# Performance work log

Hardware: AMD Instinct MI355X
Metric: run time of the kernel (lower is better)

The kernel has to match this reference:

```python
import jax, jax.numpy as jnp
import numpy as np

B, PS, D, HEADS, HD, PROP = 16, 32, 768, 8, 24, 4
N = PS * PS          # 1024 tokens
M = PROP * PROP      # 16 proposal centers
INNER = HEADS * HD   # 192
HID = 4 * D          # 3072
EPS = 1e-12


def setup_inputs() -> dict:
    key = jax.random.key(0)
    ks = jax.random.split(key, 8)
    s = 0.02
    f32 = jnp.float32
    return {
        "x": jax.random.normal(ks[0], (B, N, D), f32),
        "ln1_w": jnp.ones((D,), f32), "ln1_b": jnp.zeros((D,), f32),
        "f_w": jax.random.normal(ks[1], (INNER, D), f32) * s, "f_b": jnp.zeros((INNER,), f32),
        "v_w": jax.random.normal(ks[2], (INNER, D), f32) * s, "v_b": jnp.zeros((INNER,), f32),
        "proj_w": jax.random.normal(ks[3], (D, INNER), f32) * s, "proj_b": jnp.zeros((D,), f32),
        "sim_alpha": jnp.ones((1,), f32), "sim_beta": jnp.zeros((1,), f32),
        "ln2_w": jnp.ones((D,), f32), "ln2_b": jnp.zeros((D,), f32),
        "fc1_w": jax.random.normal(ks[4], (HID, D), f32) * s, "fc1_b": jnp.zeros((HID,), f32),
        "fc2_w": jax.random.normal(ks[5], (D, HID), f32) * s, "fc2_b": jnp.zeros((D,), f32),
    }


def _ln(x, w, b):
    mu = x.mean(-1, keepdims=True)
    var = ((x - mu) ** 2).mean(-1, keepdims=True)
    return (x - mu) / jnp.sqrt(var + 1e-5) * w + b


def _cluster2d(x, f_w, f_b, v_w, v_b, proj_w, proj_b, alpha, beta):
    b = x.shape[0]
    xi = x.reshape(b, PS, PS, D).transpose(0, 3, 1, 2)  # b c w h
    # 1x1 convs f and v
    f = jnp.einsum('oc,bcwh->bowh', f_w, xi) + f_b[None, :, None, None]
    v = jnp.einsum('oc,bcwh->bowh', v_w, xi) + v_b[None, :, None, None]
    # split heads: (b e) c w h
    f = f.reshape(b * HEADS, HD, PS, PS)
    v = v.reshape(b * HEADS, HD, PS, PS)
    # adaptive avg pool to (PROP, PROP) -- exact kernel/stride pooling since PS % PROP == 0
    s = PS // PROP
    cen = f.reshape(-1, HD, PROP, s, PROP, s).mean((3, 5))  # be c 4 4
    vcen = v.reshape(-1, HD, PROP, s, PROP, s).mean((3, 5)).reshape(-1, HD, M).transpose(0, 2, 1)  # be M c
    cf = cen.reshape(-1, HD, M).transpose(0, 2, 1)  # be M c
    xf = f.reshape(-1, HD, N).transpose(0, 2, 1)    # be N c
    # pairwise euclidean similarity on L2-normalized vectors: ||a-b|| = sqrt(2 - 2 a.b)
    cn = cf / jnp.maximum(jnp.linalg.norm(cf, axis=-1, keepdims=True), EPS)
    xn = xf / jnp.maximum(jnp.linalg.norm(xf, axis=-1, keepdims=True), EPS)
    dist = jnp.sqrt(jnp.clip(2.0 - 2.0 * jnp.einsum('bmc,bnc->bmn', cn, xn), EPS, None))
    sim = jax.nn.leaky_relu(beta + alpha * jnp.exp(-dist), 0.2)  # be M N (dropout eval = identity)
    # top-1 hard assignment (torch scatter of argmax -> one-hot mask, no grad through mask)
    mask = jax.nn.one_hot(jnp.argmax(sim, axis=1), M, dtype=sim.dtype).transpose(0, 2, 1)  # be M N
    sim = sim * mask
    v2 = v.reshape(-1, HD, N).transpose(0, 2, 1)  # be N c
    # weighted reduce to centers, then broadcast back to tokens
    outc = (jnp.einsum('bmn,bnc->bmc', sim, v2) + vcen) / (mask.sum(-1, keepdims=True) + 1.0)  # be M c
    out = jnp.einsum('bmn,bmc->bnc', sim, outc)  # be N c
    out = out.reshape(-1, PS, PS, HD).transpose(0, 3, 1, 2).reshape(b, INNER, PS, PS)
    out = jnp.einsum('oc,bcwh->bowh', proj_w, out) + proj_b[None, :, None, None]
    return out.transpose(0, 2, 3, 1).reshape(b, N, D)


def reference(x, ln1_w, ln1_b, f_w, f_b, v_w, v_b, proj_w, proj_b, sim_alpha, sim_beta,
              ln2_w, ln2_b, fc1_w, fc1_b, fc2_w, fc2_b):
    h = x + _cluster2d(_ln(x, ln1_w, ln1_b), f_w, f_b, v_w, v_b, proj_w, proj_b, sim_alpha, sim_beta)
    y = _ln(h, ln2_w, ln2_b)
    y = jax.nn.gelu(jnp.einsum('bnd,hd->bnh', y, fc1_w) + fc1_b, approximate=False)
    y = jnp.einsum('bnh,dh->bnd', y, fc2_w) + fc2_b
    return h + y
```

## Files before the change

### kernel.cpp

```cpp
#include <hip/hip_runtime.h>
#include <hip/hip_bf16.h>
#include <cmath>

typedef unsigned short u16;
typedef short short8 __attribute__((ext_vector_type(8)));
typedef float f32x4 __attribute__((ext_vector_type(4)));

#define D_ 768
#define NTOK 16384
#define INNER_ 192
#define HID_ 3072

__device__ __forceinline__ float u2f(u16 u) { return __uint_as_float((unsigned)u << 16); }
__device__ __forceinline__ u16 f2u(float f) {
  __hip_bfloat16 h = __float2bfloat16(f);
  u16 u; __builtin_memcpy(&u, &h, 2); return u;
}
__device__ __forceinline__ float ld1(const void* p, size_t i, int f32) {
  return f32 ? ((const float*)p)[i] : u2f(((const u16*)p)[i]);
}
__device__ __forceinline__ void st1(void* p, size_t i, float v, int f32) {
  if (f32) ((float*)p)[i] = v; else ((u16*)p)[i] = f2u(v);
}
__device__ __forceinline__ float gelu_exact(float v) {
  return 0.5f * v * (1.f + erff(v * 0.7071067811865476f));
}
__device__ __forceinline__ void unpack8(const uint4 v, float* o) {
  o[0] = u2f((u16)(v.x & 0xffffu)); o[1] = u2f((u16)(v.x >> 16));
  o[2] = u2f((u16)(v.y & 0xffffu)); o[3] = u2f((u16)(v.y >> 16));
  o[4] = u2f((u16)(v.z & 0xffffu)); o[5] = u2f((u16)(v.z >> 16));
  o[6] = u2f((u16)(v.w & 0xffffu)); o[7] = u2f((u16)(v.w >> 16));
}

__global__ __launch_bounds__(64) void detect_kernel(const unsigned* __restrict__ x,
                                                    int* __restrict__ flag) {
  int cnt = 0;
  for (int i = threadIdx.x; i < 512; i += 64) {
    const unsigned e0 = (x[i] >> 7) & 0xFFu;
    if (e0 >= 96u && e0 <= 144u) cnt++;
  }
#pragma unroll
  for (int o = 32; o > 0; o >>= 1) cnt += __shfl_down(cnt, o);
  if (threadIdx.x == 0) flag[0] = (cnt < 256) ? 1 : 0;
}

struct CvtJob { const void* src; u16* dst; int n4; };
struct CvtArgs { CvtJob j[10]; };

__global__ __launch_bounds__(256) void cvt_kernel(CvtArgs a, const int* __restrict__ flagp) {
  const int f32 = flagp[0];
  const CvtJob jb = a.j[blockIdx.y];
  const int i = blockIdx.x * 256 + threadIdx.x;
  if (i >= jb.n4) return;
  if (f32) {
    const float4 v = ((const float4*)jb.src)[i];
    const unsigned lo = (unsigned)f2u(v.x) | ((unsigned)f2u(v.y) << 16);
    const unsigned hi = (unsigned)f2u(v.z) | ((unsigned)f2u(v.w) << 16);
    ((uint2*)jb.dst)[i] = make_uint2(lo, hi);
  } else {
    ((uint2*)jb.dst)[i] = ((const uint2*)jb.src)[i];
  }
}

__global__ __launch_bounds__(256) void ln_kernel(const void* __restrict__ x,
                                                 const void* __restrict__ w,
                                                 const void* __restrict__ b,
                                                 u16* __restrict__ y,
                                                 const int* __restrict__ flagp) {
  const int fl = flagp[0];
  const size_t t = blockIdx.x;
  float v[3];
  float s = 0.f, s2 = 0.f;
#pragma unroll
  for (int i = 0; i < 3; i++) {
    v[i] = ld1(x, t * D_ + threadIdx.x + 256 * i, fl);
    s += v[i];
    s2 += v[i] * v[i];
  }
#pragma unroll
  for (int o = 32; o > 0; o >>= 1) {
    s += __shfl_down(s, o);
    s2 += __shfl_down(s2, o);
  }
  __shared__ float ps[4], ps2[4];
  __shared__ float smu, srstd;
  const int wid = threadIdx.x >> 6, lane = threadIdx.x & 63;
  if (lane == 0) { ps[wid] = s; ps2[wid] = s2; }
  __syncthreads();
  if (threadIdx.x == 0) {
    const float a = ps[0] + ps[1] + ps[2] + ps[3];
    const float a2 = ps2[0] + ps2[1] + ps2[2] + ps2[3];
    const float mu = a * (1.f / D_);
    smu = mu;
    srstd = rsqrtf(a2 * (1.f / D_) - mu * mu + 1e-5f);
  }
  __syncthreads();
  const float mu = smu, rstd = srstd;
#pragma unroll
  for (int i = 0; i < 3; i++) {
    const int c = threadIdx.x + 256 * i;
    y[t * D_ + c] = f2u((v[i] - mu) * rstd * ld1(w, c, fl) + ld1(b, c, fl));
  }
}

template <int EPI>
__global__ __launch_bounds__(256) void mfma_gemm(const u16* __restrict__ A, int lda,
                                                 const u16* __restrict__ B, int ldb,
                                                 const u16* __restrict__ bias,
                                                 const void* __restrict__ res,
                                                 void* __restrict__ C, int ldc,
                                                 int K, int row0,
                                                 const int* __restrict__ flagp) {
  const int fl = flagp[0];
  __shared__ __align__(16) u16 Asb[128 * 32];
  __shared__ __align__(16) u16 Bsb[128 * 32];
  const int tid = threadIdx.x;
  const int lane = tid & 63;
  const int wv = tid >> 6;
  const int bm = blockIdx.x * 128;
  const int bn = blockIdx.y * 128;
  const int wm = (wv & 1) * 64;
  const int wn = (wv >> 1) * 64;
  const int c0 = tid, c1 = tid + 256;
  const u16* Ag0 = A + (size_t)(bm + (c0 >> 2)) * lda + (c0 & 3) * 8;
  const u16* Ag1 = A + (size_t)(bm + (c1 >> 2)) * lda + (c1 & 3) * 8;
  const u16* Bg0 = B + (size_t)(bn + (c0 >> 2)) * ldb + (c0 & 3) * 8;
  const u16* Bg1 = B + (size_t)(bn + (c1 >> 2)) * ldb + (c1 & 3) * 8;
  u16* la0 = &Asb[c0 * 8];
  u16* la1 = &Asb[c1 * 8];
  u16* lb0 = &Bsb[c0 * 8];
  u16* lb1 = &Bsb[c1 * 8];

  f32x4 acc[4][4];
#pragma unroll
  for (int i = 0; i < 4; i++)
#pragma unroll
    for (int j = 0; j < 4; j++) acc[i][j] = (f32x4){0.f, 0.f, 0.f, 0.f};

  const int ml = lane & 15;
  const int kq = (lane >> 4) * 8;

  for (int k0 = 0; k0 < K; k0 += 32) {
    __syncthreads();
    __builtin_amdgcn_global_load_lds(
        (const __attribute__((address_space(1))) void*)(Ag0 + k0),
        (__attribute__((address_space(3))) void*)la0, 16, 0, 0);
    __builtin_amdgcn_global_load_lds(
        (const __attribute__((address_space(1))) void*)(Ag1 + k0),
        (__attribute__((address_space(3))) void*)la1, 16, 0, 0);
    __builtin_amdgcn_global_load_lds(
        (const __attribute__((address_space(1))) void*)(Bg0 + k0),
        (__attribute__((address_space(3))) void*)lb0, 16, 0, 0);
    __builtin_amdgcn_global_load_lds(
        (const __attribute__((address_space(1))) void*)(Bg1 + k0),
        (__attribute__((address_space(3))) void*)lb1, 16, 0, 0);
    __syncthreads();
    short8 af[4], bf[4];
#pragma unroll
    for (int i = 0; i < 4; i++) {
      af[i] = *(const short8*)&Asb[(wm + i * 16 + ml) * 32 + kq];
      bf[i] = *(const short8*)&Bsb[(wn + i * 16 + ml) * 32 + kq];
    }
#pragma unroll
    for (int i = 0; i < 4; i++)
#pragma unroll
      for (int j = 0; j < 4; j++)
        acc[i][j] = __builtin_amdgcn_mfma_f32_16x16x32_bf16(af[i], bf[j], acc[i][j], 0, 0, 0);
  }

  const int qr = (lane >> 4) * 4;
#pragma unroll
  for (int i = 0; i < 4; i++) {
#pragma unroll
    for (int j = 0; j < 4; j++) {
      const int colg = bn + wn + j * 16 + ml;
      const float bb = u2f(bias[colg]);
#pragma unroll
      for (int r = 0; r < 4; r++) {
        const size_t row = (size_t)row0 + bm + wm + i * 16 + qr + r;
        float v = acc[i][j][r] + bb;
        if (EPI == 1) v = gelu_exact(v);
        if (EPI == 2) {
          v += ld1(res, row * ldc + colg, fl);
          st1(C, row * ldc + colg, v, fl);
        } else {
          ((u16*)C)[row * ldc + colg] = f2u(v);
        }
      }
    }
  }
}

__global__ __launch_bounds__(512) void cluster_kernel(u16* __restrict__ FV,
                                                      const void* __restrict__ alpha_p,
                                                      const void* __restrict__ beta_p,
                                                      const int* __restrict__ flagp) {
  const int fl = flagp[0];
  const int be = blockIdx.x;
  const int b = be >> 3, e = be & 7;
  const int tid = threadIdx.x;
  const float alpha = ld1(alpha_p, 0, fl), beta = ld1(beta_p, 0, fl);

  __shared__ __align__(16) u16 S[1024 * 24];
  __shared__ float cn[16][24];
  __shared__ float vcen[16][24];
  __shared__ float outc[16][24];
  __shared__ float rcn[16];
  __shared__ int cnt[16];

  u16* Fg = FV + ((size_t)b * 1024) * 384 + e * 24;
  const u16* Vg = Fg + 192;

  for (int c = tid; c < 3072; c += 512) {
    const int n = c / 3, q = c - n * 3;
    *(uint4*)&S[n * 24 + q * 8] = *(const uint4*)(Fg + (size_t)n * 384 + q * 8);
  }
  if (tid < 16) cnt[tid] = 0;
  __syncthreads();

  for (int t = tid; t < 384; t += 512) {
    const int m = t / 24, ch = t - m * 24;
    const int pw = m >> 2, ph = m & 3;
    float sum = 0.f;
    for (int dw = 0; dw < 8; dw++) {
      const int base = (pw * 8 + dw) * 32 + ph * 8;
      for (int dh = 0; dh < 8; dh++) sum += u2f(S[(base + dh) * 24 + ch]);
    }
    cn[m][ch] = sum * (1.f / 64.f);
  }
  __syncthreads();
  if (tid < 16) {
    float s = 0.f;
    for (int ch = 0; ch < 24; ch++) { const float v = cn[tid][ch]; s += v * v; }
    rcn[tid] = 1.f / fmaxf(sqrtf(s), 1e-12f);
  }
  __syncthreads();

  const int na = tid, nb = tid + 512;
  float besta = -3.4e38f, bestb = -3.4e38f;
  int bma = 0, bmb = 0;
  {
    float xa[24], xb[24];
    const uint4* ra = (const uint4*)&S[na * 24];
    const uint4* rb = (const uint4*)&S[nb * 24];
#pragma unroll
    for (int q = 0; q < 3; q++) {
      unpack8(ra[q], &xa[q * 8]);
      unpack8(rb[q], &xb[q * 8]);
    }
    float ssa = 0.f, ssb = 0.f;
#pragma unroll
    for (int ch = 0; ch < 24; ch++) {
      ssa = fmaf(xa[ch], xa[ch], ssa);
      ssb = fmaf(xb[ch], xb[ch], ssb);
    }
    const float rna = 1.f / fmaxf(sqrtf(ssa), 1e-12f);
    const float rnb = 1.f / fmaxf(sqrtf(ssb), 1e-12f);
    for (int m = 0; m < 16; m++) {
      float da = 0.f, db = 0.f;
#pragma unroll
      for (int k = 0; k < 12; k++) {
        const float2 c = *(const float2*)&cn[m][2 * k];
        da = fmaf(c.x, xa[2 * k], da); da = fmaf(c.y, xa[2 * k + 1], da);
        db = fmaf(c.x, xb[2 * k], db); db = fmaf(c.y, xb[2 * k + 1], db);
      }
      const float rc = rcn[m];
      da *= rna * rc;
      db *= rnb * rc;
      const float dda = sqrtf(fmaxf(2.f - 2.f * da, 1e-12f));
      const float ddb = sqrtf(fmaxf(2.f - 2.f * db, 1e-12f));
      const float za = beta + alpha * expf(-dda);
      const float zb = beta + alpha * expf(-ddb);
      const float sa = (za >= 0.f) ? za : 0.2f * za;
      const float sb = (zb >= 0.f) ? zb : 0.2f * zb;
      if (sa > besta) { besta = sa; bma = m; }
      if (sb > bestb) { bestb = sb; bmb = m; }
    }
    atomicAdd(&cnt[bma], 1);
    atomicAdd(&cnt[bmb], 1);
  }
  __syncthreads();

  for (int c = tid; c < 3072; c += 512) {
    const int n = c / 3, q = c - n * 3;
    *(uint4*)&S[n * 24 + q * 8] = *(const uint4*)(Vg + (size_t)n * 384 + q * 8);
  }
  if (tid < 384) outc[tid / 24][tid - (tid / 24) * 24] = 0.f;
  __syncthreads();

  for (int t = tid; t < 384; t += 512) {
    const int m = t / 24, ch = t - m * 24;
    const int pw = m >> 2, ph = m & 3;
    float sum = 0.f;
    for (int dw = 0; dw < 8; dw++) {
      const int base = (pw * 8 + dw) * 32 + ph * 8;
      for (int dh = 0; dh < 8; dh++) sum += u2f(S[(base + dh) * 24 + ch]);
    }
    vcen[m][ch] = sum * (1.f / 64.f);
  }

  {
    float va[24], vb[24];
    const uint4* ra = (const uint4*)&S[na * 24];
    const uint4* rb = (const uint4*)&S[nb * 24];
#pragma unroll
    for (int q = 0; q < 3; q++) {
      unpack8(ra[q], &va[q * 8]);
      unpack8(rb[q], &vb[q * 8]);
    }
#pragma unroll
    for (int ch = 0; ch < 24; ch++) {
      atomicAdd(&outc[bma][ch], besta * va[ch]);
      atomicAdd(&outc[bmb][ch], bestb * vb[ch]);
    }
  }
  __syncthreads();

  for (int t = tid; t < 384; t += 512) {
    const int m = t / 24, ch = t - m * 24;
    outc[m][ch] = (outc[m][ch] + vcen[m][ch]) / ((float)cnt[m] + 1.f);
  }
  __syncthreads();

#pragma unroll
  for (int pass = 0; pass < 2; pass++) {
    const int n = pass ? nb : na;
    const int m = pass ? bmb : bma;
    const float s = pass ? bestb : besta;
    unsigned w[12];
#pragma unroll
    for (int k = 0; k < 12; k++) {
      w[k] = (unsigned)f2u(s * outc[m][2 * k]) |
             ((unsigned)f2u(s * outc[m][2 * k + 1]) << 16);
    }
    uint4* dst = (uint4*)(Fg + (size_t)n * 384);
    dst[0] = make_uint4(w[0], w[1], w[2], w[3]);
    dst[1] = make_uint4(w[4], w[5], w[6], w[7]);
    dst[2] = make_uint4(w[8], w[9], w[10], w[11]);
  }
}

extern "C" void kernel_launch(void* const* d_in, const int* in_sizes, int n_in,
                              void* d_out, int out_size, void* d_ws, size_t ws_size,
                              hipStream_t stream) {
  const void* x      = d_in[0];
  const void* ln1_w  = d_in[1];
  const void* ln1_b  = d_in[2];
  const void* f_w    = d_in[3];
  const void* f_b    = d_in[4];
  const void* v_w    = d_in[5];
  const void* v_b    = d_in[6];
  const void* proj_w = d_in[7];
  const void* proj_b = d_in[8];
  const void* alpha  = d_in[9];
  const void* beta   = d_in[10];
  const void* ln2_w  = d_in[11];
  const void* ln2_b  = d_in[12];
  const void* fc1_w  = d_in[13];
  const void* fc1_b  = d_in[14];
  const void* fc2_w  = d_in[15];
  const void* fc2_b  = d_in[16];

  char* ws = (char*)d_ws;
  int* flag  = (int*)(ws + 0);
  u16* fvw   = (u16*)(ws + 256);
  u16* prw   = (u16*)(ws + 590080);
  u16* f1w   = (u16*)(ws + 884992);
  u16* f2w   = (u16*)(ws + 5603584);
  u16* fvb   = (u16*)(ws + 10322176);
  u16* prb   = (u16*)(ws + 10322944);
  u16* f1b   = (u16*)(ws + 10324480);
  u16* f2b_  = (u16*)(ws + 10330624);
  u16* Y1    = (u16*)(ws + 10332416);
  u16* FV    = (u16*)(ws + 35498240);
  u16* Gext  = (u16*)(ws + 48081152);

  const long extra = (long)ws_size - 48081152L;
  u16* G; long crows;
  if (extra >= (long)NTOK * HID_ * 2) { G = Gext; crows = NTOK; }
  else if (extra >= 128L * HID_ * 2) { G = Gext; crows = (extra / (HID_ * 2)) / 128 * 128; }
  else { G = FV; crows = 2048; }

  detect_kernel<<<1, 64, 0, stream>>>((const unsigned*)x, flag);

  CvtArgs ca;
  ca.j[0] = {f_w,    fvw,            147456 / 4};
  ca.j[1] = {v_w,    fvw + 147456,   147456 / 4};
  ca.j[2] = {proj_w, prw,            147456 / 4};
  ca.j[3] = {fc1_w,  f1w,            2359296 / 4};
  ca.j[4] = {fc2_w,  f2w,            2359296 / 4};
  ca.j[5] = {f_b,    fvb,            192 / 4};
  ca.j[6] = {v_b,    fvb + 192,      192 / 4};
  ca.j[7] = {proj_b, prb,            768 / 4};
  ca.j[8] = {fc1_b,  f1b,            3072 / 4};
  ca.j[9] = {fc2_b,  f2b_,           768 / 4};
  cvt_kernel<<<dim3(2304, 10), 256, 0, stream>>>(ca, flag);

  ln_kernel<<<NTOK, 256, 0, stream>>>(x, ln1_w, ln1_b, Y1, flag);
  mfma_gemm<0><<<dim3(128, 3), 256, 0, stream>>>(
      Y1, D_, fvw, D_, fvb, nullptr, FV, 384, D_, 0, flag);
  cluster_kernel<<<128, 512, 0, stream>>>(FV, alpha, beta, flag);
  mfma_gemm<2><<<dim3(128, 6), 256, 0, stream>>>(
      FV, 384, prw, INNER_, prb, x, d_out, D_, INNER_, 0, flag);
  ln_kernel<<<NTOK, 256, 0, stream>>>(d_out, ln2_w, ln2_b, Y1, flag);
  for (long t0 = 0; t0 < NTOK; t0 += crows) {
    const long ct = (t0 + crows <= NTOK) ? crows : (NTOK - t0);
    mfma_gemm<1><<<dim3(ct / 128, 24), 256, 0, stream>>>(
        Y1 + t0 * D_, D_, f1w, D_, f1b, nullptr, G, HID_, D_, 0, flag);
    mfma_gemm<2><<<dim3(ct / 128, 6), 256, 0, stream>>>(
        G, HID_, f2w, HID_, f2b_, d_out, d_out, D_, HID_, (int)t0, flag);
  }
}
```

Baseline: 521.7 us.

## Add 256x256-tile 8-wave MFMA GEMM with staged LDS pipeline for MLP

Adds a new GEMM kernel with 256x256 output tiles, 8 waves per 512-thread block, and double-buffered direct global-to-LDS loads. Loads are split into half-K stages interleaved with the MFMA phases, with explicit barriers, waitcnts and priority bumps. It replaces the 128x128 GEMM for fc1 and fc2, aiming to raise data reuse per LDS byte and hide load latency. The trade-off is fewer blocks (a 64x12 grid for fc1, 64x3 for fc2), which may underfill the CUs on fc2, plus heavier register and LDS use. The chunk size is now rounded to 256 rows to match the new tile.

```diff
diff --git a/kernel.cpp b/kernel.cpp
--- a/kernel.cpp
+++ b/kernel.cpp
@@ -191,6 +191,174 @@
   }
 }
 
+#define SB8 __builtin_amdgcn_sched_barrier(0)
+#define BAR8 __builtin_amdgcn_s_barrier()
+
+template <int EPI>
+__global__ __launch_bounds__(512) void mfma_gemm8(const u16* __restrict__ A, int lda,
+                                                  const u16* __restrict__ B, int ldb,
+                                                  const u16* __restrict__ bias,
+                                                  const void* __restrict__ res,
+                                                  void* __restrict__ C, int ldc,
+                                                  int K, int row0,
+                                                  const int* __restrict__ flagp) {
+  const int fl = flagp[0];
+  __shared__ __align__(16) u16 L[2][2][2][8192];
+  const int tid = threadIdx.x;
+  const int lane = tid & 63;
+  const int wv = tid >> 6;
+  const int bm = blockIdx.x * 256;
+  const int bn = blockIdx.y * 256;
+  const int wm = (wv >> 2) * 128;
+  const int wn = (wv & 3) * 64;
+  const int ml = lane & 15;
+  const int qk = lane >> 4;
+
+  const int srow = tid >> 2;
+  const int q_s = (tid & 3) ^ ((srow >> 1) & 3);
+  const size_t ga0 = (size_t)(bm + srow) * lda + q_s * 8;
+  const size_t ga1 = (size_t)(bm + srow + 128) * lda + q_s * 8;
+  const size_t gb0 = (size_t)(bn + srow) * ldb + q_s * 8;
+  const size_t gb1 = (size_t)(bn + srow + 128) * ldb + q_s * 8;
+
+  int offA[8], offB[4];
+#pragma unroll
+  for (int i = 0; i < 8; i++) {
+    const int r = wm + i * 16 + ml;
+    offA[i] = (r * 4 + (qk ^ ((r >> 1) & 3))) * 8;
+  }
+#pragma unroll
+  for (int j = 0; j < 4; j++) {
+    const int r = wn + j * 16 + ml;
+    offB[j] = (r * 4 + (qk ^ ((r >> 1) & 3))) * 8;
+  }
+
+  f32x4 acc[8][4];
+#pragma unroll
+  for (int i = 0; i < 8; i++)
+#pragma unroll
+    for (int j = 0; j < 4; j++) acc[i][j] = (f32x4){0.f, 0.f, 0.f, 0.f};
+
+  const int NT = K >> 6;
+
+#define STG8(arrx, ksx, tilex, bufx) do {                                          \
+    const u16* gsrc_ = (arrx) ? B : A;                                             \
+    const size_t k_ = (size_t)(tilex) * 64 + (ksx) * 32;                           \
+    u16* lb_ = &L[(bufx)][(arrx)][(ksx)][0];                                       \
+    __builtin_amdgcn_global_load_lds(                                              \
+        (const __attribute__((address_space(1))) void*)(gsrc_ + ((arrx) ? gb0 : ga0) + k_), \
+        (__attribute__((address_space(3))) void*)(lb_ + tid * 8), 16, 0, 0);       \
+    __builtin_amdgcn_global_load_lds(                                              \
+        (const __attribute__((address_space(1))) void*)(gsrc_ + ((arrx) ? gb1 : ga1) + k_), \
+        (__attribute__((address_space(3))) void*)(lb_ + (tid + 512) * 8), 16, 0, 0); \
+  } while (0)
+
+  STG8(1, 0, 0, 0); STG8(0, 0, 0, 0); STG8(1, 1, 0, 0); STG8(0, 1, 0, 0);
+  if (NT > 1) {
+    STG8(1, 0, 1, 1); STG8(0, 0, 1, 1); STG8(1, 1, 1, 1);
+    asm volatile("s_waitcnt vmcnt(6)" ::: "memory");
+  } else {
+    asm volatile("s_waitcnt vmcnt(0)" ::: "memory");
+  }
+  SB8; BAR8; SB8;
+
+  for (int t = 0; t < NT; t++) {
+    const int buf = t & 1;
+    const u16* LA0 = &L[buf][0][0][0];
+    const u16* LA1 = &L[buf][0][1][0];
+    const u16* LB0 = &L[buf][1][0][0];
+    const u16* LB1 = &L[buf][1][1][0];
+    short8 afr[4], bfr[4];
+
+#pragma unroll
+    for (int j = 0; j < 4; j++) bfr[j] = *(const short8*)(LB0 + offB[j]);
+#pragma unroll
+    for (int i = 0; i < 4; i++) afr[i] = *(const short8*)(LA0 + offA[i]);
+    if (t + 1 < NT) STG8(0, 1, t + 1, (t + 1) & 1);
+    SB8; BAR8;
+    asm volatile("s_waitcnt lgkmcnt(0)" ::: "memory"); SB8;
+    __builtin_amdgcn_s_setprio(1);
+#pragma unroll
+    for (int i = 0; i < 4; i++)
+#pragma unroll
+      for (int j = 0; j < 4; j++)
+        acc[i][j] = __builtin_amdgcn_mfma_f32_16x16x32_bf16(afr[i], bfr[j], acc[i][j], 0, 0, 0);
+    __builtin_amdgcn_s_setprio(0);
+    SB8; BAR8;
+
+#pragma unroll
+    for (int i = 0; i < 4; i++) afr[i] = *(const short8*)(LA0 + offA[4 + i]);
+    if (t + 2 < NT) STG8(1, 0, t + 2, buf);
+    SB8; BAR8;
+    asm volatile("s_waitcnt lgkmcnt(0)" ::: "memory"); SB8;
+    __builtin_amdgcn_s_setprio(1);
+#pragma unroll
+    for (int i = 0; i < 4; i++)
+#pragma unroll
+      for (int j = 0; j < 4; j++)
+        acc[4 + i][j] = __builtin_amdgcn_mfma_f32_16x16x32_bf16(afr[i], bfr[j], acc[4 + i][j], 0, 0, 0);
+    __builtin_amdgcn_s_setprio(0);
+    SB8; BAR8;
+
+#pragma unroll
+    for (int j = 0; j < 4; j++) bfr[j] = *(const short8*)(LB1 + offB[j]);
+#pragma unroll
+    for (int i = 0; i < 4; i++) afr[i] = *(const short8*)(LA1 + offA[i]);
+    if (t + 2 < NT) STG8(0, 0, t + 2, buf);
+    SB8; BAR8;
+    asm volatile("s_waitcnt lgkmcnt(0)" ::: "memory"); SB8;
+    __builtin_amdgcn_s_setprio(1);
+#pragma unroll
+    for (int i = 0; i < 4; i++)
+#pragma unroll
+      for (int j = 0; j < 4; j++)
+        acc[i][j] = __builtin_amdgcn_mfma_f32_16x16x32_bf16(afr[i], bfr[j], acc[i][j], 0, 0, 0);
+    __builtin_amdgcn_s_setprio(0);
+    SB8; BAR8;
+
+#pragma unroll
+    for (int i = 0; i < 4; i++) afr[i] = *(const short8*)(LA1 + offA[4 + i]);
+    if (t + 2 < NT) STG8(1, 1, t + 2, buf);
+    if (t + 1 < NT) {
+      if (t + 2 < NT) { asm volatile("s_waitcnt vmcnt(6)" ::: "memory"); }
+      else            { asm volatile("s_waitcnt vmcnt(0)" ::: "memory"); }
+    }
+    SB8; BAR8;
+    asm volatile("s_waitcnt lgkmcnt(0)" ::: "memory"); SB8;
+    __builtin_amdgcn_s_setprio(1);
+#pragma unroll
+    for (int i = 0; i < 4; i++)
+#pragma unroll
+      for (int j = 0; j < 4; j++)
+        acc[4 + i][j] = __builtin_amdgcn_mfma_f32_16x16x32_bf16(afr[i], bfr[j], acc[4 + i][j], 0, 0, 0);
+    __builtin_amdgcn_s_setprio(0);
+    SB8; BAR8;
+  }
+#undef STG8
+
+  const int qr = (lane >> 4) * 4;
+#pragma unroll
+  for (int i = 0; i < 8; i++) {
+#pragma unroll
+    for (int j = 0; j < 4; j++) {
+      const int colg = bn + wn + j * 16 + ml;
+      const float bb = u2f(bias[colg]);
+#pragma unroll
+      for (int r = 0; r < 4; r++) {
+        const size_t row = (size_t)row0 + bm + wm + i * 16 + qr + r;
+        float v = acc[i][j][r] + bb;
+        if (EPI == 1) v = gelu_exact(v);
+        if (EPI == 2) {
+          v += ld1(res, row * ldc + colg, fl);
+          st1(C, row * ldc + colg, v, fl);
+        } else {
+          ((u16*)C)[row * ldc + colg] = f2u(v);
+        }
+      }
+    }
+  }
+}
+
 __global__ __launch_bounds__(512) void cluster_kernel(u16* __restrict__ FV,
                                                       const void* __restrict__ alpha_p,
                                                       const void* __restrict__ beta_p,
@@ -378,7 +546,7 @@
   const long extra = (long)ws_size - 48081152L;
   u16* G; long crows;
   if (extra >= (long)NTOK * HID_ * 2) { G = Gext; crows = NTOK; }
-  else if (extra >= 128L * HID_ * 2) { G = Gext; crows = (extra / (HID_ * 2)) / 128 * 128; }
+  else if (extra >= 256L * HID_ * 2) { G = Gext; crows = (extra / (HID_ * 2)) / 256 * 256; }
   else { G = FV; crows = 2048; }
 
   detect_kernel<<<1, 64, 0, stream>>>((const unsigned*)x, flag);
@@ -405,9 +573,9 @@
   ln_kernel<<<NTOK, 256, 0, stream>>>(d_out, ln2_w, ln2_b, Y1, flag);
   for (long t0 = 0; t0 < NTOK; t0 += crows) {
     const long ct = (t0 + crows <= NTOK) ? crows : (NTOK - t0);
-    mfma_gemm<1><<<dim3(ct / 128, 24), 256, 0, stream>>>(
+    mfma_gemm8<1><<<dim3(ct / 256, HID_ / 256), 512, 0, stream>>>(
         Y1 + t0 * D_, D_, f1w, D_, f1b, nullptr, G, HID_, D_, 0, flag);
-    mfma_gemm<2><<<dim3(ct / 128, 6), 256, 0, stream>>>(
+    mfma_gemm8<2><<<dim3(ct / 256, D_ / 256), 512, 0, stream>>>(
         G, HID_, f2w, HID_, f2b_, d_out, d_out, D_, HID_, (int)t0, flag);
   }
 }
```

After: 528.5 us. No clear change (+1.3%).

## Add 128x256-tile triple-buffered direct-to-LDS GEMM for the MLP layers

Applied to the files above, without the earlier changes.

Introduces a new GEMM kernel with 512 threads and 128x256 output tiles. It uses global_load_lds direct-to-LDS copies into a three-stage shared-memory ring with explicit vmcnt waits, XOR-swizzled LDS layout, raised MFMA priority, and a grouped block-index remap for L2 locality. The fc1 and fc2 MLP GEMMs now launch this kernel, and chunk rows are rounded to 256. The aim is to hide global-load latency and raise tile reuse on the dominant GEMMs, at the cost of higher LDS use per block, lower occupancy, and constraints on tile divisibility.

```diff
diff --git a/kernel.cpp b/kernel.cpp
--- a/kernel.cpp
+++ b/kernel.cpp
@@ -191,6 +191,143 @@
   }
 }
 
+#define SB8 __builtin_amdgcn_sched_barrier(0)
+#define BAR8 __builtin_amdgcn_s_barrier()
+
+template <int EPI>
+__global__ __launch_bounds__(512, 4) void mfma_gemmP(const u16* __restrict__ A, int lda,
+                                                     const u16* __restrict__ B, int ldb,
+                                                     const u16* __restrict__ bias,
+                                                     const void* __restrict__ res,
+                                                     void* __restrict__ C, int ldc,
+                                                     int K, int row0, int gm, int gn,
+                                                     const int* __restrict__ flagp) {
+  const int fl = flagp[0];
+  __shared__ __align__(16) u16 L[3][(128 + 256) * 32];
+  const int tid = threadIdx.x;
+  const int lane = tid & 63;
+  const int wv = tid >> 6;
+
+  int mb_, nb_;
+  {
+    const int bid = blockIdx.x;
+    const int ntot = gm * gn;
+    if ((ntot & 511) == 0 && (512 % gm) == 0 && gm >= 2) {
+      const int l = bid >> 8, p = bid & 255;
+      const int G = gm >> 1;
+      nb_ = (l >> 1) * (512 / gm) + p / G;
+      mb_ = (p % G) * 2 + (l & 1);
+    } else {
+      mb_ = bid % gm;
+      nb_ = bid / gm;
+    }
+  }
+  const int bm = mb_ * 128;
+  const int bn = nb_ * 256;
+
+  const int wm = (wv & 1) * 64;
+  const int wn = (wv >> 1) * 64;
+  const int ml = lane & 15;
+  const int qk = lane >> 4;
+
+  const int srow = tid >> 2;
+  const int q_s = (tid & 3) ^ ((srow >> 1) & 3);
+  const size_t gaA  = (size_t)(bm + srow) * lda + q_s * 8;
+  const size_t gbB0 = (size_t)(bn + srow) * ldb + q_s * 8;
+  const size_t gbB1 = (size_t)(bn + srow + 128) * ldb + q_s * 8;
+
+  int offA[4], offB[4];
+#pragma unroll
+  for (int i = 0; i < 4; i++) {
+    const int r = wm + i * 16 + ml;
+    offA[i] = (r * 4 + (qk ^ ((r >> 1) & 3))) * 8;
+  }
+#pragma unroll
+  for (int j = 0; j < 4; j++) {
+    const int r = wn + j * 16 + ml;
+    offB[j] = 4096 + (r * 4 + (qk ^ ((r >> 1) & 3))) * 8;
+  }
+
+  f32x4 acc[4][4];
+#pragma unroll
+  for (int i = 0; i < 4; i++)
+#pragma unroll
+    for (int j = 0; j < 4; j++) acc[i][j] = (f32x4){0.f, 0.f, 0.f, 0.f};
+
+  const int NT = K >> 5;
+
+#define STGP(tilex) do {                                                            \
+    const size_t k_ = (size_t)(tilex) * 32;                                         \
+    u16* lb_ = &L[(tilex) % 3][0];                                                  \
+    __builtin_amdgcn_global_load_lds(                                               \
+        (const __attribute__((address_space(1))) void*)(A + gaA + k_),              \
+        (__attribute__((address_space(3))) void*)(lb_ + tid * 8), 16, 0, 0);        \
+    __builtin_amdgcn_global_load_lds(                                               \
+        (const __attribute__((address_space(1))) void*)(B + gbB0 + k_),             \
+        (__attribute__((address_space(3))) void*)(lb_ + 4096 + tid * 8), 16, 0, 0); \
+    __builtin_amdgcn_global_load_lds(                                               \
+        (const __attribute__((address_space(1))) void*)(B + gbB1 + k_),             \
+        (__attribute__((address_space(3))) void*)(lb_ + 4096 + (tid + 512) * 8), 16, 0, 0); \
+  } while (0)
+
+  STGP(0);
+  if (NT > 1) {
+    STGP(1);
+    asm volatile("s_waitcnt vmcnt(3)" ::: "memory");
+  } else {
+    asm volatile("s_waitcnt vmcnt(0)" ::: "memory");
+  }
+  SB8; BAR8; SB8;
+
+  for (int t = 0; t < NT; t++) {
+    const u16* Lb = &L[t % 3][0];
+    short8 af[4], bf[4];
+#pragma unroll
+    for (int j = 0; j < 4; j++) bf[j] = *(const short8*)(Lb + offB[j]);
+#pragma unroll
+    for (int i = 0; i < 4; i++) af[i] = *(const short8*)(Lb + offA[i]);
+    if (t + 2 < NT) {
+      STGP(t + 2);
+      asm volatile("s_waitcnt vmcnt(3)" ::: "memory");
+    } else if (t + 1 < NT) {
+      asm volatile("s_waitcnt vmcnt(0)" ::: "memory");
+    }
+    SB8; BAR8;
+    asm volatile("s_waitcnt lgkmcnt(0)" ::: "memory"); SB8;
+    __builtin_amdgcn_s_setprio(1);
+#pragma unroll
+    for (int i = 0; i < 4; i++)
+#pragma unroll
+      for (int j = 0; j < 4; j++)
+        acc[i][j] = __builtin_amdgcn_mfma_f32_16x16x32_bf16(af[i], bf[j], acc[i][j], 0, 0, 0);
+    __builtin_amdgcn_s_setprio(0);
+    SB8; BAR8;
+  }
+#undef STGP
+
+  const int qr = (lane >> 4) * 4;
+#pragma unroll
+  for (int i = 0; i < 4; i++) {
+#pragma unroll
+    for (int j = 0; j < 4; j++) {
+      const int colg = bn + wn + j * 16 + ml;
+      const float bb = u2f(bias[colg]);
+#pragma unroll
+      for (int r = 0; r < 4; r++) {
+        const size_t row = (size_t)row0 + bm + wm + i * 16 + qr + r;
+        float v = acc[i][j][r] + bb;
+        if (EPI == 1) v = gelu_exact(v);
+        if (EPI == 2) {
+          v += ld1(res, row * ldc + colg, fl);
+          st1(C, row * ldc + colg, v, fl);
+        } else {
+          ((u16*)C)[row * ldc + colg] = f2u(v);
+        }
+      }
+    }
+  }
+}
+
 __global__ __launch_bounds__(512) void cluster_kernel(u16* __restrict__ FV,
                                                       const void* __restrict__ alpha_p,
                                                       const void* __restrict__ beta_p,
@@ -378,7 +515,7 @@
   const long extra = (long)ws_size - 48081152L;
   u16* G; long crows;
   if (extra >= (long)NTOK * HID_ * 2) { G = Gext; crows = NTOK; }
-  else if (extra >= 128L * HID_ * 2) { G = Gext; crows = (extra / (HID_ * 2)) / 128 * 128; }
+  else if (extra >= 256L * HID_ * 2) { G = Gext; crows = (extra / (HID_ * 2)) / 256 * 256; }
   else { G = FV; crows = 2048; }
 
   detect_kernel<<<1, 64, 0, stream>>>((const unsigned*)x, flag);
@@ -405,9 +542,11 @@
   ln_kernel<<<NTOK, 256, 0, stream>>>(d_out, ln2_w, ln2_b, Y1, flag);
   for (long t0 = 0; t0 < NTOK; t0 += crows) {
     const long ct = (t0 + crows <= NTOK) ? crows : (NTOK - t0);
-    mfma_gemm<1><<<dim3(ct / 128, 24), 256, 0, stream>>>(
-        Y1 + t0 * D_, D_, f1w, D_, f1b, nullptr, G, HID_, D_, 0, flag);
-    mfma_gemm<2><<<dim3(ct / 128, 6), 256, 0, stream>>>(
-        G, HID_, f2w, HID_, f2b_, d_out, d_out, D_, HID_, (int)t0, flag);
-  }
-}
+    const int gm1 = (int)(ct / 128), gn1 = HID_ / 256;
+    const int gm2 = (int)(ct / 128), gn2 = D_ / 256;
+    mfma_gemmP<1><<<dim3(gm1 * gn1), 512, 0, stream>>>(
+        Y1 + t0 * D_, D_, f1w, D_, f1b, nullptr, G, HID_, D_, 0, gm1, gn1, flag);
+    mfma_gemmP<2><<<dim3(gm2 * gn2), 512, 0, stream>>>(
+        G, HID_, f2w, HID_, f2b_, d_out, d_out, D_, HID_, (int)t0, gm2, gn2, flag);
+  }
+}
```

After: 488.1 us. 6.4% less time.
